# Optimization experiments

Hardware: AMD Instinct MI355X
Metric: run time of the kernel (lower is better)

## Reference

```python
import jax, jax.numpy as jnp
import numpy as np

N = 50000   # nodes of ntype 'A'
E = 800000  # edges per metapath
M = 4       # metapaths (first-order, tail = 'A')
H = 4       # attn heads
C = 32      # out_channels = output_dim // attn_heads
IN = 256    # input_dim
D = H * C   # output_dim = 128
NEG_SLOPE = 0.2


def setup_inputs() -> dict:
    key = jax.random.key(0)
    ks = jax.random.split(key, 8)
    feats = jax.random.normal(ks[0], (N, IN), dtype=jnp.float32)
    edge_index = jax.random.randint(ks[1], (M, 2, E), 0, N, dtype=jnp.int32)
    W = jax.random.normal(ks[2], (IN, D), dtype=jnp.float32) * (2.0 / (IN + D)) ** 0.5
    b = jnp.zeros((D,), dtype=jnp.float32)
    attn = jax.random.normal(ks[3], (M, H, 2 * C), dtype=jnp.float32) * 0.1
    rel_attn_l = jax.random.normal(ks[4], (H, C), dtype=jnp.float32) * 0.1
    rel_attn_r = jax.random.normal(ks[5], (M + 1, H, C), dtype=jnp.float32) * 0.1
    rel_attn_bias = jnp.zeros((M + 1,), dtype=jnp.float32)
    return {"feats": feats, "edge_index": edge_index, "W": W, "b": b,
            "attn": attn, "rel_attn_l": rel_attn_l, "rel_attn_r": rel_attn_r,
            "rel_attn_bias": rel_attn_bias}


def _segment_softmax(logits, seg, num_segments):
    # logits: [E, H], seg: [E] target-node ids; softmax over incoming edges per node.
    seg_max = jax.ops.segment_max(logits, seg, num_segments=num_segments)  # [N, H]
    e = jnp.exp(logits - seg_max[seg])
    seg_sum = jax.ops.segment_sum(e, seg, num_segments=num_segments)       # [N, H]
    return e / (seg_sum[seg] + 1e-16)


def reference(feats, edge_index, W, b, attn, rel_attn_l, rel_attn_r, rel_attn_bias):
    # projection: per-ntype Linear + relu, reshape to heads
    h = jax.nn.relu(feats @ W + b).reshape(N, H, C)  # l_dict == r_dict == h

    # per-metapath GAT-style propagate (aggr='add')
    rels = []
    for m in range(M):
        src = edge_index[m, 0]
        dst = edge_index[m, 1]
        x_j = h[src]  # [E, H, C] source messages
        x_i = h[dst]  # [E, H, C] target queries
        # alpha = (cat([x_i, x_j], -1) * attn[m]).sum(-1), LeakyReLU(0.2)
        logits = jnp.einsum('ehc,hc->eh', x_i, attn[m, :, :C]) \
               + jnp.einsum('ehc,hc->eh', x_j, attn[m, :, C:])
        logits = jax.nn.leaky_relu(logits, NEG_SLOPE)
        alpha = _segment_softmax(logits, dst, N)                 # [E, H]
        out = jax.ops.segment_sum(x_j * alpha[..., None], dst, num_segments=N)  # [N, H, C]
        rels.append(out)
    rels.append(h)  # last relation slot = self (embedding[:, -1] = l_dict[ntype])
    emb = jnp.stack(rels, axis=1)  # [N, M+1, H, C]

    # beta relation-attention weights
    beta_l = jax.nn.relu(h * rel_attn_l)                          # [N, H, C]
    beta_r = jax.nn.relu(emb * rel_attn_r)                        # [N, M+1, H, C]
    beta = jnp.einsum('nhc,nrhc->nrh', beta_l, beta_r) + rel_attn_bias[None, :, None]
    beta = jax.nn.softmax(beta, axis=1)                           # over relations

    emb = (emb * beta[..., None]).sum(axis=1).reshape(N, D)
    return jax.nn.relu(emb)
```

## Files before the change

kernel.cpp:

```cpp
#include <hip/hip_runtime.h>
#include <math.h>

#define kN 50000
#define kE 800000
#define kM 4
#define kH 4
#define kC 32
#define kIN 256
#define kD 128

typedef __attribute__((ext_vector_type(8))) short bf16x8;
typedef __attribute__((ext_vector_type(4))) float f32x4;

__device__ __forceinline__ unsigned int f2bf_pack(float a, float b) {
    unsigned ua = __float_as_uint(a);
    ua += 0x7fffu + ((ua >> 16) & 1u);
    unsigned ub = __float_as_uint(b);
    ub += 0x7fffu + ((ub >> 16) & 1u);
    return (ua >> 16) | (ub & 0xffff0000u);
}
__device__ __forceinline__ unsigned short f2bf(float x) {
    unsigned u = __float_as_uint(x);
    u += 0x7fffu + ((u >> 16) & 1u);
    return (unsigned short)(u >> 16);
}

#define NBK 98
#define BCAP 10240
#define MW (NBK * BCAP)
#define PAB ((kE + 4095) / 4096)

__global__ void k_wcast(const float* __restrict__ W, unsigned short* __restrict__ Wt16) {
    const int col = blockIdx.x;
    const int k = threadIdx.x;
    Wt16[(size_t)col * kIN + k] = f2bf(W[(size_t)k * kD + col]);
}

#define GEMMB ((kN + 127) / 128)
__global__ __launch_bounds__(256) void k_gemmbucket(const float* __restrict__ feats,
                                                    const unsigned short* __restrict__ Wt16,
                                                    const float* __restrict__ b,
                                                    unsigned short* __restrict__ h16,
                                                    const int* __restrict__ ei,
                                                    int* __restrict__ bcur,
                                                    unsigned int* __restrict__ pairs) {
    __shared__ unsigned short fr16[128 * 32];
    __shared__ int hist[NBK], h2[NBK], base_s[NBK];
    const int t = threadIdx.x;

    if (blockIdx.x >= GEMMB) {
        const int bi = blockIdx.x - GEMMB;
        const int m = bi / PAB;
        const int chunk = bi - m * PAB;
        const int e0 = chunk * 4096;
        for (int j = t; j < NBK; j += 256) { hist[j] = 0; h2[j] = 0; }
        __syncthreads();
        int src[16], dst[16];
#pragma unroll
        for (int i = 0; i < 16; i++) {
            const int e = e0 + i * 256 + t;
            const int eok = (e < kE) ? e : 0;
            src[i] = ei[(size_t)m * 2 * kE + eok];
            dst[i] = (e < kE) ? ei[(size_t)m * 2 * kE + kE + eok] : -1;
        }
#pragma unroll
        for (int i = 0; i < 16; i++)
            if (dst[i] >= 0) atomicAdd(&hist[dst[i] >> 9], 1);
        __syncthreads();
        for (int j = t; j < NBK; j += 256)
            base_s[j] = atomicAdd(&bcur[m * NBK + j], hist[j]);
        __syncthreads();
#pragma unroll
        for (int i = 0; i < 16; i++) {
            if (dst[i] >= 0) {
                const int bk = dst[i] >> 9;
                const int slot = base_s[bk] + atomicAdd(&h2[bk], 1);
                pairs[(size_t)m * MW + (size_t)bk * BCAP + slot] =
                    ((unsigned int)(dst[i] & 511) << 16) | (unsigned int)src[i];
            }
        }
        return;
    }

    const int lane = t & 63;
    const int wave = t >> 6;
    const int q = lane >> 4;
    const int m16 = lane & 15;
    const int wrow = (wave >> 1) * 64;
    const int wcol = (wave & 1) * 64;
    const int rowbase = blockIdx.x * 128;

    f32x4 acc[4][4];
#pragma unroll
    for (int i = 0; i < 4; i++)
#pragma unroll
        for (int j = 0; j < 4; j++) acc[i][j] = (f32x4){0.f, 0.f, 0.f, 0.f};

    const int srow = t >> 3;
    const int sk4 = t & 7;

    for (int kc = 0; kc < kIN; kc += 32) {
        __syncthreads();
#pragma unroll
        for (int it = 0; it < 4; it++) {
            const int row = srow + it * 32;
            const int rg = rowbase + row;
            float4 v = make_float4(0.f, 0.f, 0.f, 0.f);
            if (rg < kN)
                v = *reinterpret_cast<const float4*>(feats + (size_t)rg * kIN + kc + sk4 * 4);
            uint2 p;
            p.x = f2bf_pack(v.x, v.y);
            p.y = f2bf_pack(v.z, v.w);
            *reinterpret_cast<uint2*>(&fr16[row * 32 + sk4 * 4]) = p;
        }
        __syncthreads();

        bf16x8 afr[4], bfr[4];
#pragma unroll
        for (int ri = 0; ri < 4; ri++)
            afr[ri] = *reinterpret_cast<const bf16x8*>(
                &fr16[(wrow + ri * 16 + m16) * 32 + q * 8]);
#pragma unroll
        for (int ci = 0; ci < 4; ci++)
            bfr[ci] = *reinterpret_cast<const bf16x8*>(
                Wt16 + (size_t)(wcol + ci * 16 + m16) * kIN + kc + q * 8);
#pragma unroll
        for (int ri = 0; ri < 4; ri++)
#pragma unroll
            for (int ci = 0; ci < 4; ci++)
                acc[ri][ci] = __builtin_amdgcn_mfma_f32_16x16x32_bf16(
                    afr[ri], bfr[ci], acc[ri][ci], 0, 0, 0);
    }

    float bcol[4];
#pragma unroll
    for (int ci = 0; ci < 4; ci++) bcol[ci] = b[wcol + ci * 16 + m16];

#pragma unroll
    for (int ri = 0; ri < 4; ri++) {
#pragma unroll
        for (int reg = 0; reg < 4; reg++) {
            const int row = rowbase + wrow + ri * 16 + q * 4 + reg;
            if (row < kN) {
#pragma unroll
                for (int ci = 0; ci < 4; ci++) {
                    const int col = wcol + ci * 16 + m16;
                    const float v = fmaxf(acc[ri][ci][reg] + bcol[ci], 0.f);
                    h16[(size_t)row * kD + col] = f2bf(v);
                }
            }
        }
    }
}

#define SORTB (kM * NBK)
#define SLRB ((kN * kH + 255) / 256)
__global__ __launch_bounds__(256) void k_sortslr(const unsigned int* __restrict__ pairs,
                                                 const int* __restrict__ bcur,
                                                 int* __restrict__ offs,
                                                 int* __restrict__ cnta,
                                                 int* __restrict__ srcsort,
                                                 const unsigned short* __restrict__ h16,
                                                 const float* __restrict__ attn,
                                                 float* __restrict__ sl,
                                                 float* __restrict__ sr) {
    const int t = threadIdx.x;
    if (blockIdx.x < SORTB) {
        __shared__ int hist[512], pref[512], h2[512], wt[4];
        const int m = blockIdx.x / NBK;
        const int bk = blockIdx.x - m * NBK;
        const int bs = bk << 9;
        const int base = bk * BCAP;
        const int n = bcur[m * NBK + bk];
        const unsigned int* __restrict__ pb = pairs + (size_t)m * MW + base;
        int* __restrict__ ss = srcsort + (size_t)m * MW + base;

        hist[t] = 0; hist[t + 256] = 0; h2[t] = 0; h2[t + 256] = 0;
        __syncthreads();

        for (int c0 = 0; c0 < n; c0 += 2048) {
            unsigned int v[8]; bool ok[8];
#pragma unroll
            for (int j = 0; j < 8; j++) {
                const int idx = c0 + j * 256 + t;
                ok[j] = idx < n;
                v[j] = pb[ok[j] ? idx : 0];
            }
#pragma unroll
            for (int j = 0; j < 8; j++)
                if (ok[j]) atomicAdd(&hist[v[j] >> 16], 1);
        }
        __syncthreads();

        const int lane = t & 63, wid = t >> 6;
        const int j0 = 2 * t, j1 = 2 * t + 1;
        const int h0 = hist[j0], h1 = hist[j1];
        const int s = h0 + h1;
        int incl = s;
#pragma unroll
        for (int d = 1; d < 64; d <<= 1) {
            const int x = __shfl_up(incl, d);
            if (lane >= d) incl += x;
        }
        if (lane == 63) wt[wid] = incl;
        __syncthreads();
        int woff = 0;
#pragma unroll
        for (int i = 0; i < 4; i++)
            if (i < wid) woff += wt[i];
        const int excl = woff + incl - s;
        pref[j0] = excl;
        pref[j1] = excl + h0;
        const int d0 = bs + j0, d1 = bs + j1;
        if (d0 < kN) { offs[m * kN + d0] = base + excl;       cnta[m * kN + d0] = h0; }
        if (d1 < kN) { offs[m * kN + d1] = base + excl + h0;  cnta[m * kN + d1] = h1; }
        __syncthreads();

        for (int c0 = 0; c0 < n; c0 += 2048) {
            unsigned int v[8]; bool ok[8];
#pragma unroll
            for (int j = 0; j < 8; j++) {
                const int idx = c0 + j * 256 + t;
                ok[j] = idx < n;
                v[j] = pb[ok[j] ? idx : 0];
            }
#pragma unroll
            for (int j = 0; j < 8; j++) {
                if (ok[j]) {
                    const int dl = (int)(v[j] >> 16);
                    const int pos = pref[dl] + atomicAdd(&h2[dl], 1);
                    ss[pos] = (int)(v[j] & 0xffffu);
                }
            }
        }
        return;
    }
    const int id = (blockIdx.x - SORTB) * 256 + t;
    if (id >= kN * kH) return;
    const int n = id >> 2;
    const int hh = id & 3;
    const unsigned int* hu =
        reinterpret_cast<const unsigned int*>(h16 + (size_t)n * kD + hh * kC);
    unsigned int u[16];
    uint4 u4;
#pragma unroll
    for (int i = 0; i < 4; i++) {
        u4 = reinterpret_cast<const uint4*>(hu)[i];
        u[i * 4 + 0] = u4.x; u[i * 4 + 1] = u4.y; u[i * 4 + 2] = u4.z; u[i * 4 + 3] = u4.w;
    }
    float f0[16], f1[16];
#pragma unroll
    for (int c = 0; c < 16; c++) {
        f0[c] = __uint_as_float(u[c] << 16);
        f1[c] = __uint_as_float(u[c] & 0xffff0000u);
    }
#pragma unroll
    for (int m = 0; m < kM; m++) {
        const float2* al = reinterpret_cast<const float2*>(attn + (m * kH + hh) * 2 * kC);
        const float2* ar = al + 16;
        float s0 = 0.f, s1 = 0.f;
#pragma unroll
        for (int c = 0; c < 16; c++) {
            const float2 a = al[c], r = ar[c];
            s0 += f0[c] * a.x + f1[c] * a.y;
            s1 += f0[c] * r.x + f1[c] * r.y;
        }
        sl[((size_t)m * kN + n) * kH + hh] = s0;
        sr[((size_t)m * kN + n) * kH + hh] = s1;
    }
}

#define CH 16

#define AGG_BODY(GN)                                                            \
    {                                                                           \
        int sj[GN];                                                             \
        _Pragma("unroll")                                                       \
        for (int j = 0; j < GN; j++) {                                          \
            const int id = __builtin_amdgcn_readlane(my0, j);                   \
            sj[j] = (j < nb) ? id : dst;                                        \
        }                                                                       \
        unsigned int u[GN];                                                     \
        _Pragma("unroll")                                                       \
        for (int j = 0; j < GN; j++)                                            \
            u[j] = *reinterpret_cast<const unsigned int*>(                      \
                hb + (((size_t)(unsigned int)sj[j] << 8) + ebyte));             \
        float x = sl_h + srv;                                                   \
        x = x > 0.f ? x : 0.2f * x;                         \
        const float w = (c + jj < cnt) ? __expf(x) : 0.f;                       \
        sum += w;                                                               \
        swts[m][l] = w;                                                         \
        __builtin_amdgcn_wave_barrier();                                        \
        const float4 w0 = *reinterpret_cast<const float4*>(&swts[m][hh * 16]);  \
        const float4 w1 = *reinterpret_cast<const float4*>(&swts[m][hh*16+4]);  \
        const float4 w2 = *reinterpret_cast<const float4*>(&swts[m][hh*16+8]);  \
        const float4 w3 = *reinterpret_cast<const float4*>(&swts[m][hh*16+12]); \
        __builtin_amdgcn_wave_barrier();                                        \
        my0 = my1;                                                              \
        my1 = sbase[c + 2 * CH + jj];                                           \
        srv = *reinterpret_cast<const float*>(                                  \
            srb + (((unsigned int)my0 << 4) + hbyte));                          \
        const float wj[16] = {w0.x, w0.y, w0.z, w0.w, w1.x, w1.y, w1.z, w1.w,   \
                              w2.x, w2.y, w2.z, w2.w, w3.x, w3.y, w3.z, w3.w};  \
        _Pragma("unroll")                                                       \
        for (int j = 0; j < GN; j++) {                                          \
            a0 += wj[j] * __uint_as_float(u[j] << 16);                          \
            a1 += wj[j] * __uint_as_float(u[j] & 0xffff0000u);                  \
        }                                                                       \
    }

__global__ __launch_bounds__(256) void k_agg(const unsigned short* __restrict__ h16,
                                             const float* __restrict__ sl,
                                             const float* __restrict__ sr,
                                             const int* __restrict__ offs,
                                             const int* __restrict__ cnta,
                                             const int* __restrict__ srcsort,
                                             const float* __restrict__ ral,
                                             const float* __restrict__ rar,
                                             const float* __restrict__ rbias,
                                             float* __restrict__ out) {
    const int dst = blockIdx.x;
    const int t = threadIdx.x;
    const int m = t >> 6;
    const int l = t & 63;
    const int hh = l >> 4;
    const int jj = l & 15;
    const int e0 = l * 2;

    __shared__ float smres[kM][kD];
    __shared__ float swts[kM][64];

    const int beg = offs[m * kN + dst];
    const int cnt = cnta[m * kN + dst];
    const float sl_h = sl[((size_t)m * kN + dst) * kH + hh];
    const int* __restrict__ sbase = srcsort + (size_t)m * MW + beg;
    const char* __restrict__ hb = (const char*)h16;
    const char* __restrict__ srb = (const char*)(sr + (size_t)m * kN * kH);
    const unsigned int ebyte = (unsigned int)(e0 << 1);
    const unsigned int hbyte = (unsigned int)(hh << 2);

    float sum = 0.f, a0 = 0.f, a1 = 0.f;

    int my0 = sbase[jj];
    int my1 = sbase[CH + jj];
    float srv = *reinterpret_cast<const float*>(
        srb + (((unsigned int)my0 << 4) + hbyte));

    for (int c = 0; c < cnt; c += CH) {
        const int nb = cnt - c;
        if (nb >= 9) AGG_BODY(16) else AGG_BODY(8)
    }

    sum += __shfl_xor(sum, 1);
    sum += __shfl_xor(sum, 2);
    sum += __shfl_xor(sum, 4);
    sum += __shfl_xor(sum, 8);
    const float inv = 1.0f / (sum + 1e-16f);
    smres[m][e0] = a0 * inv;
    smres[m][e0 + 1] = a1 * inv;
    __syncthreads();

    if (m == 0) {
        const unsigned int ud = *reinterpret_cast<const unsigned int*>(
            hb + (((unsigned int)dst << 8) + ebyte));
        const float hd0 = __uint_as_float(ud << 16);
        const float hd1 = __uint_as_float(ud & 0xffff0000u);
        const float bl0 = fmaxf(hd0 * ral[e0], 0.f);
        const float bl1 = fmaxf(hd1 * ral[e0 + 1], 0.f);
        float emb0[5], emb1[5], beta[5];
#pragma unroll
        for (int r = 0; r < 5; r++) {
            const float x0 = (r < 4) ? smres[r][e0] : hd0;
            const float x1 = (r < 4) ? smres[r][e0 + 1] : hd1;
            emb0[r] = x0;
            emb1[r] = x1;
            const float br0 = fmaxf(x0 * rar[r * kD + e0], 0.f);
            const float br1 = fmaxf(x1 * rar[r * kD + e0 + 1], 0.f);
            float p = bl0 * br0 + bl1 * br1;
            p += __shfl_xor(p, 1);
            p += __shfl_xor(p, 2);
            p += __shfl_xor(p, 4);
            p += __shfl_xor(p, 8);
            beta[r] = p + rbias[r];
        }
        float mx = beta[0];
#pragma unroll
        for (int r = 1; r < 5; r++) mx = fmaxf(mx, beta[r]);
        float s = 0.f, wgt[5];
#pragma unroll
        for (int r = 0; r < 5; r++) { wgt[r] = __expf(beta[r] - mx); s += wgt[r]; }
        const float invb = 1.f / s;
        float o0 = 0.f, o1 = 0.f;
#pragma unroll
        for (int r = 0; r < 5; r++) { o0 += emb0[r] * wgt[r]; o1 += emb1[r] * wgt[r]; }
        out[(size_t)dst * kD + e0] = fmaxf(o0 * invb, 0.f);
        out[(size_t)dst * kD + e0 + 1] = fmaxf(o1 * invb, 0.f);
    }
}

extern "C" void kernel_launch(void* const* d_in, const int* in_sizes, int n_in,
                              void* d_out, int out_size, void* d_ws, size_t ws_size,
                              hipStream_t stream) {
    const float* feats = (const float*)d_in[0];
    const int* ei      = (const int*)d_in[1];
    const float* W     = (const float*)d_in[2];
    const float* b     = (const float*)d_in[3];
    const float* attn  = (const float*)d_in[4];
    const float* ral   = (const float*)d_in[5];
    const float* rar   = (const float*)d_in[6];
    const float* rbias = (const float*)d_in[7];
    float* out = (float*)d_out;

    char* ws = (char*)d_ws;
    size_t off = 0;
    auto alloc = [&](size_t bytes) -> void* {
        void* p = ws + off;
        off = (off + bytes + 255) & ~(size_t)255;
        return p;
    };
    unsigned short* h16 = (unsigned short*)alloc(sizeof(short) * (size_t)kN * kD);
    unsigned short* Wt16= (unsigned short*)alloc(sizeof(short) * (size_t)kD * kIN);
    float* sl   = (float*)alloc(sizeof(float) * (size_t)kM * kN * kH);
    float* sr   = (float*)alloc(sizeof(float) * (size_t)kM * kN * kH);
    int* cnta   = (int*)alloc(sizeof(int) * (size_t)kM * kN);
    int* offs   = (int*)alloc(sizeof(int) * (size_t)kM * kN);
    int* bcur   = (int*)alloc(sizeof(int) * (kM * NBK + 64));
    int* srcsort= (int*)alloc(sizeof(int) * ((size_t)kM * MW + 64));
    unsigned int* pairs = (unsigned int*)alloc(sizeof(int) * (size_t)kM * MW);

    hipMemsetAsync(bcur, 0, sizeof(int) * (kM * NBK + 64), stream);
    hipMemsetAsync(srcsort, 0, sizeof(int) * ((size_t)kM * MW + 64), stream);
    k_wcast<<<kD, kIN, 0, stream>>>(W, Wt16);
    k_gemmbucket<<<GEMMB + kM * PAB, 256, 0, stream>>>(feats, Wt16, b, h16, ei,
                                                       bcur, pairs);
    k_sortslr<<<SORTB + SLRB, 256, 0, stream>>>(pairs, bcur, offs, cnta, srcsort,
                                                h16, attn, sl, sr);
    k_agg<<<kN, 256, 0, stream>>>(h16, sl, sr, offs, cnta, srcsort,
                                  ral, rar, rbias, out);
}
```

Measured before the change: 347.8 us.

## Fuse attention score compute into GEMM epilogue, register-resident sort, two dsts per agg block

```diff
diff --git a/kernel.cpp b/kernel.cpp
--- a/kernel.cpp
+++ b/kernel.cpp
@@ -40,11 +40,15 @@
 __global__ __launch_bounds__(256) void k_gemmbucket(const float* __restrict__ feats,
                                                     const unsigned short* __restrict__ Wt16,
                                                     const float* __restrict__ b,
+                                                    const float* __restrict__ attn,
                                                     unsigned short* __restrict__ h16,
+                                                    float* __restrict__ sl,
+                                                    float* __restrict__ sr,
                                                     const int* __restrict__ ei,
                                                     int* __restrict__ bcur,
                                                     unsigned int* __restrict__ pairs) {
     __shared__ unsigned short fr16[128 * 32];
+    __shared__ unsigned short hlds[128][130];
     __shared__ int hist[NBK], h2[NBK], base_s[NBK];
     const int t = threadIdx.x;
 
@@ -140,133 +144,117 @@
     for (int ri = 0; ri < 4; ri++) {
 #pragma unroll
         for (int reg = 0; reg < 4; reg++) {
-            const int row = rowbase + wrow + ri * 16 + q * 4 + reg;
-            if (row < kN) {
-#pragma unroll
-                for (int ci = 0; ci < 4; ci++) {
-                    const int col = wcol + ci * 16 + m16;
-                    const float v = fmaxf(acc[ri][ci][reg] + bcol[ci], 0.f);
-                    h16[(size_t)row * kD + col] = f2bf(v);
+            const int row = wrow + ri * 16 + q * 4 + reg;
+            const int rg = rowbase + row;
+#pragma unroll
+            for (int ci = 0; ci < 4; ci++) {
+                const int col = wcol + ci * 16 + m16;
+                const float v = fmaxf(acc[ri][ci][reg] + bcol[ci], 0.f);
+                const unsigned short us = f2bf(v);
+                hlds[row][col] = us;
+                if (rg < kN)
+                    h16[(size_t)rg * kD + col] = us;
+            }
+        }
+    }
+    __syncthreads();
+
+    const unsigned int* hl32 = reinterpret_cast<const unsigned int*>(&hlds[0][0]);
+#pragma unroll
+    for (int it = 0; it < 2; it++) {
+        const int task = it * 256 + t;
+        const int hh = task >> 7;
+        const int nl = task & 127;
+        const int n = rowbase + nl;
+        if (n < kN) {
+            unsigned int u[16];
+#pragma unroll
+            for (int k = 0; k < 16; k++) u[k] = hl32[nl * 65 + hh * 16 + k];
+            float f0[16], f1[16];
+#pragma unroll
+            for (int k = 0; k < 16; k++) {
+                f0[k] = __uint_as_float(u[k] << 16);
+                f1[k] = __uint_as_float(u[k] & 0xffff0000u);
+            }
+#pragma unroll
+            for (int m = 0; m < kM; m++) {
+                const float2* al = reinterpret_cast<const float2*>(attn + (m * kH + hh) * 2 * kC);
+                const float2* ar = al + 16;
+                float s0 = 0.f, s1 = 0.f;
+#pragma unroll
+                for (int k = 0; k < 16; k++) {
+                    const float2 a = al[k], r = ar[k];
+                    s0 += f0[k] * a.x + f1[k] * a.y;
+                    s1 += f0[k] * r.x + f1[k] * r.y;
                 }
+                sl[(size_t)(m * kH + hh) * kN + n] = s0;
+                sr[(size_t)(m * kH + hh) * kN + n] = s1;
             }
         }
     }
 }
 
 #define SORTB (kM * NBK)
-#define SLRB ((kN * kH + 255) / 256)
-__global__ __launch_bounds__(256) void k_sortslr(const unsigned int* __restrict__ pairs,
-                                                 const int* __restrict__ bcur,
-                                                 int* __restrict__ offs,
-                                                 int* __restrict__ cnta,
-                                                 int* __restrict__ srcsort,
-                                                 const unsigned short* __restrict__ h16,
-                                                 const float* __restrict__ attn,
-                                                 float* __restrict__ sl,
-                                                 float* __restrict__ sr) {
+__global__ __launch_bounds__(256) void k_sort(const unsigned int* __restrict__ pairs,
+                                              const int* __restrict__ bcur,
+                                              int* __restrict__ offs,
+                                              int* __restrict__ cnta,
+                                              int* __restrict__ srcsort) {
+    __shared__ int hist[512], pref[512], h2[512], wt[4];
     const int t = threadIdx.x;
-    if (blockIdx.x < SORTB) {
-        __shared__ int hist[512], pref[512], h2[512], wt[4];
-        const int m = blockIdx.x / NBK;
-        const int bk = blockIdx.x - m * NBK;
-        const int bs = bk << 9;
-        const int base = bk * BCAP;
-        const int n = bcur[m * NBK + bk];
-        const unsigned int* __restrict__ pb = pairs + (size_t)m * MW + base;
-        int* __restrict__ ss = srcsort + (size_t)m * MW + base;
-
-        hist[t] = 0; hist[t + 256] = 0; h2[t] = 0; h2[t + 256] = 0;
-        __syncthreads();
-
-        for (int c0 = 0; c0 < n; c0 += 2048) {
-            unsigned int v[8]; bool ok[8];
-#pragma unroll
-            for (int j = 0; j < 8; j++) {
-                const int idx = c0 + j * 256 + t;
-                ok[j] = idx < n;
-                v[j] = pb[ok[j] ? idx : 0];
-            }
-#pragma unroll
-            for (int j = 0; j < 8; j++)
-                if (ok[j]) atomicAdd(&hist[v[j] >> 16], 1);
-        }
-        __syncthreads();
-
-        const int lane = t & 63, wid = t >> 6;
-        const int j0 = 2 * t, j1 = 2 * t + 1;
-        const int h0 = hist[j0], h1 = hist[j1];
-        const int s = h0 + h1;
-        int incl = s;
-#pragma unroll
-        for (int d = 1; d < 64; d <<= 1) {
-            const int x = __shfl_up(incl, d);
-            if (lane >= d) incl += x;
-        }
-        if (lane == 63) wt[wid] = incl;
-        __syncthreads();
-        int woff = 0;
-#pragma unroll
-        for (int i = 0; i < 4; i++)
-            if (i < wid) woff += wt[i];
-        const int excl = woff + incl - s;
-        pref[j0] = excl;
-        pref[j1] = excl + h0;
-        const int d0 = bs + j0, d1 = bs + j1;
-        if (d0 < kN) { offs[m * kN + d0] = base + excl;       cnta[m * kN + d0] = h0; }
-        if (d1 < kN) { offs[m * kN + d1] = base + excl + h0;  cnta[m * kN + d1] = h1; }
-        __syncthreads();
-
-        for (int c0 = 0; c0 < n; c0 += 2048) {
-            unsigned int v[8]; bool ok[8];
-#pragma unroll
-            for (int j = 0; j < 8; j++) {
-                const int idx = c0 + j * 256 + t;
-                ok[j] = idx < n;
-                v[j] = pb[ok[j] ? idx : 0];
-            }
-#pragma unroll
-            for (int j = 0; j < 8; j++) {
-                if (ok[j]) {
-                    const int dl = (int)(v[j] >> 16);
-                    const int pos = pref[dl] + atomicAdd(&h2[dl], 1);
-                    ss[pos] = (int)(v[j] & 0xffffu);
-                }
-            }
-        }
-        return;
-    }
-    const int id = (blockIdx.x - SORTB) * 256 + t;
-    if (id >= kN * kH) return;
-    const int n = id >> 2;
-    const int hh = id & 3;
-    const unsigned int* hu =
-        reinterpret_cast<const unsigned int*>(h16 + (size_t)n * kD + hh * kC);
-    unsigned int u[16];
-    uint4 u4;
-#pragma unroll
-    for (int i = 0; i < 4; i++) {
-        u4 = reinterpret_cast<const uint4*>(hu)[i];
-        u[i * 4 + 0] = u4.x; u[i * 4 + 1] = u4.y; u[i * 4 + 2] = u4.z; u[i * 4 + 3] = u4.w;
-    }
-    float f0[16], f1[16];
-#pragma unroll
-    for (int c = 0; c < 16; c++) {
-        f0[c] = __uint_as_float(u[c] << 16);
-        f1[c] = __uint_as_float(u[c] & 0xffff0000u);
-    }
-#pragma unroll
-    for (int m = 0; m < kM; m++) {
-        const float2* al = reinterpret_cast<const float2*>(attn + (m * kH + hh) * 2 * kC);
-        const float2* ar = al + 16;
-        float s0 = 0.f, s1 = 0.f;
-#pragma unroll
-        for (int c = 0; c < 16; c++) {
-            const float2 a = al[c], r = ar[c];
-            s0 += f0[c] * a.x + f1[c] * a.y;
-            s1 += f0[c] * r.x + f1[c] * r.y;
-        }
-        sl[((size_t)m * kN + n) * kH + hh] = s0;
-        sr[((size_t)m * kN + n) * kH + hh] = s1;
+    const int m = blockIdx.x / NBK;
+    const int bk = blockIdx.x - m * NBK;
+    const int bs = bk << 9;
+    const int base = bk * BCAP;
+    const int n = bcur[m * NBK + bk];
+    const unsigned int* __restrict__ pb = pairs + (size_t)m * MW + base;
+    int* __restrict__ ss = srcsort + (size_t)m * MW + base;
+
+    hist[t] = 0; hist[t + 256] = 0; h2[t] = 0; h2[t + 256] = 0;
+    __syncthreads();
+
+    unsigned int v[40];
+#pragma unroll
+    for (int j = 0; j < 40; j++) {
+        const int idx = j * 256 + t;
+        v[j] = (idx < n) ? pb[idx] : 0xffffffffu;
+    }
+#pragma unroll
+    for (int j = 0; j < 40; j++)
+        if (v[j] != 0xffffffffu) atomicAdd(&hist[v[j] >> 16], 1);
+    __syncthreads();
+
+    const int lane = t & 63, wid = t >> 6;
+    const int j0 = 2 * t, j1 = 2 * t + 1;
+    const int h0 = hist[j0], h1 = hist[j1];
+    const int s = h0 + h1;
+    int incl = s;
+#pragma unroll
+    for (int d = 1; d < 64; d <<= 1) {
+        const int x = __shfl_up(incl, d);
+        if (lane >= d) incl += x;
+    }
+    if (lane == 63) wt[wid] = incl;
+    __syncthreads();
+    int woff = 0;
+#pragma unroll
+    for (int i = 0; i < 4; i++)
+        if (i < wid) woff += wt[i];
+    const int excl = woff + incl - s;
+    pref[j0] = excl;
+    pref[j1] = excl + h0;
+    const int d0 = bs + j0, d1 = bs + j1;
+    if (d0 < kN) { offs[m * kN + d0] = base + excl;       cnta[m * kN + d0] = h0; }
+    if (d1 < kN) { offs[m * kN + d1] = base + excl + h0;  cnta[m * kN + d1] = h1; }
+    __syncthreads();
+
+#pragma unroll
+    for (int j = 0; j < 40; j++) {
+        if (v[j] != 0xffffffffu) {
+            const int dl = (int)(v[j] >> 16);
+            const int pos = pref[dl] + atomicAdd(&h2[dl], 1);
+            ss[pos] = (int)(v[j] & 0xffffu);
+        }
     }
 }
 
@@ -289,17 +277,16 @@
         x = x > 0.f ? x : 0.2f * x;                         \
         const float w = (c + jj < cnt) ? __expf(x) : 0.f;                       \
         sum += w;                                                               \
-        swts[m][l] = w;                                                         \
+        swtsH[m][l] = w;                                                        \
         __builtin_amdgcn_wave_barrier();                                        \
-        const float4 w0 = *reinterpret_cast<const float4*>(&swts[m][hh * 16]);  \
-        const float4 w1 = *reinterpret_cast<const float4*>(&swts[m][hh*16+4]);  \
-        const float4 w2 = *reinterpret_cast<const float4*>(&swts[m][hh*16+8]);  \
-        const float4 w3 = *reinterpret_cast<const float4*>(&swts[m][hh*16+12]); \
+        const float4 w0 = *reinterpret_cast<const float4*>(&swtsH[m][hh * 16]); \
+        const float4 w1 = *reinterpret_cast<const float4*>(&swtsH[m][hh*16+4]); \
+        const float4 w2 = *reinterpret_cast<const float4*>(&swtsH[m][hh*16+8]); \
+        const float4 w3 = *reinterpret_cast<const float4*>(&swtsH[m][hh*16+12]);\
         __builtin_amdgcn_wave_barrier();                                        \
         my0 = my1;                                                              \
         my1 = sbase[c + 2 * CH + jj];                                           \
-        srv = *reinterpret_cast<const float*>(                                  \
-            srb + (((unsigned int)my0 << 4) + hbyte));                          \
+        srv = srb[my0];                                                         \
         const float wj[16] = {w0.x, w0.y, w0.z, w0.w, w1.x, w1.y, w1.z, w1.w,   \
                               w2.x, w2.y, w2.z, w2.w, w3.x, w3.y, w3.z, w3.w};  \
         _Pragma("unroll")                                                       \
@@ -309,7 +296,7 @@
         }                                                                       \
     }
 
-__global__ __launch_bounds__(256) void k_agg(const unsigned short* __restrict__ h16,
+__global__ __launch_bounds__(512) void k_agg(const unsigned short* __restrict__ h16,
                                              const float* __restrict__ sl,
                                              const float* __restrict__ sr,
                                              const int* __restrict__ offs,
@@ -319,32 +306,33 @@
                                              const float* __restrict__ rar,
                                              const float* __restrict__ rbias,
                                              float* __restrict__ out) {
-    const int dst = blockIdx.x;
     const int t = threadIdx.x;
-    const int m = t >> 6;
+    const int hv = t >> 8;
+    const int dst = blockIdx.x * 2 + hv;
+    const int m = (t >> 6) & 3;
     const int l = t & 63;
     const int hh = l >> 4;
     const int jj = l & 15;
     const int e0 = l * 2;
 
-    __shared__ float smres[kM][kD];
-    __shared__ float swts[kM][64];
+    __shared__ float smres[2][kM][kD];
+    __shared__ float swts[2][kM][64];
+    float (* __restrict__ smresH)[kD] = smres[hv];
+    float (* __restrict__ swtsH)[64] = swts[hv];
 
     const int beg = offs[m * kN + dst];
     const int cnt = cnta[m * kN + dst];
-    const float sl_h = sl[((size_t)m * kN + dst) * kH + hh];
+    const float sl_h = sl[(size_t)(m * kH + hh) * kN + dst];
     const int* __restrict__ sbase = srcsort + (size_t)m * MW + beg;
     const char* __restrict__ hb = (const char*)h16;
-    const char* __restrict__ srb = (const char*)(sr + (size_t)m * kN * kH);
+    const float* __restrict__ srb = sr + (size_t)(m * kH + hh) * kN;
     const unsigned int ebyte = (unsigned int)(e0 << 1);
-    const unsigned int hbyte = (unsigned int)(hh << 2);
 
     float sum = 0.f, a0 = 0.f, a1 = 0.f;
 
     int my0 = sbase[jj];
     int my1 = sbase[CH + jj];
-    float srv = *reinterpret_cast<const float*>(
-        srb + (((unsigned int)my0 << 4) + hbyte));
+    float srv = srb[my0];
 
     for (int c = 0; c < cnt; c += CH) {
         const int nb = cnt - c;
@@ -356,8 +344,8 @@
     sum += __shfl_xor(sum, 4);
     sum += __shfl_xor(sum, 8);
     const float inv = 1.0f / (sum + 1e-16f);
-    smres[m][e0] = a0 * inv;
-    smres[m][e0 + 1] = a1 * inv;
+    smresH[m][e0] = a0 * inv;
+    smresH[m][e0 + 1] = a1 * inv;
     __syncthreads();
 
     if (m == 0) {
@@ -370,8 +358,8 @@
         float emb0[5], emb1[5], beta[5];
 #pragma unroll
         for (int r = 0; r < 5; r++) {
-            const float x0 = (r < 4) ? smres[r][e0] : hd0;
-            const float x1 = (r < 4) ? smres[r][e0 + 1] : hd1;
+            const float x0 = (r < 4) ? smresH[r][e0] : hd0;
+            const float x1 = (r < 4) ? smresH[r][e0 + 1] : hd1;
             emb0[r] = x0;
             emb1[r] = x1;
             const float br0 = fmaxf(x0 * rar[r * kD + e0], 0.f);
@@ -431,10 +419,9 @@
     hipMemsetAsync(bcur, 0, sizeof(int) * (kM * NBK + 64), stream);
     hipMemsetAsync(srcsort, 0, sizeof(int) * ((size_t)kM * MW + 64), stream);
     k_wcast<<<kD, kIN, 0, stream>>>(W, Wt16);
-    k_gemmbucket<<<GEMMB + kM * PAB, 256, 0, stream>>>(feats, Wt16, b, h16, ei,
-                                                       bcur, pairs);
-    k_sortslr<<<SORTB + SLRB, 256, 0, stream>>>(pairs, bcur, offs, cnta, srcsort,
-                                                h16, attn, sl, sr);
-    k_agg<<<kN, 256, 0, stream>>>(h16, sl, sr, offs, cnta, srcsort,
-                                  ral, rar, rbias, out);
-}
+    k_gemmbucket<<<GEMMB + kM * PAB, 256, 0, stream>>>(feats, Wt16, b, attn,
+                                                       h16, sl, sr, ei, bcur, pairs);
+    k_sort<<<SORTB, 256, 0, stream>>>(pairs, bcur, offs, cnta, srcsort);
+    k_agg<<<kN / 2, 512, 0, stream>>>(h16, sl, sr, offs, cnta, srcsort,
+                                      ral, rar, rbias, out);
+}
```

Measured after the change: 383.9 us. 1.1x slower.
